# Kernel tuning notes

Measured on AMD Instinct MI355X. Metric: run time of the kernel, lower is better.

The kernel has to match this reference:

```python
import jax, jax.numpy as jnp
import numpy as np

EMBED = 768
HEADS = 12
HEAD_DIM = EMBED // HEADS
HIDDEN = 4 * EMBED
EPS = 1e-5


def setup_inputs() -> dict:
    key = jax.random.key(0)
    ks = jax.random.split(key, 12)
    s = lambda fan_in: 1.0 / np.sqrt(fan_in)
    return {
        "x": jax.random.normal(ks[0], (4, 2048, EMBED), dtype=jnp.float32),
        "ln1_g": jnp.ones((EMBED,), jnp.float32),
        "ln1_b": jnp.zeros((EMBED,), jnp.float32),
        "qkv_w": jax.random.normal(ks[1], (EMBED, 3 * EMBED), jnp.float32) * s(EMBED),
        "qkv_b": jnp.zeros((3 * EMBED,), jnp.float32),
        "proj_w": jax.random.normal(ks[2], (EMBED, EMBED), jnp.float32) * s(EMBED),
        "proj_b": jnp.zeros((EMBED,), jnp.float32),
        "ln2_g": jnp.ones((EMBED,), jnp.float32),
        "ln2_b": jnp.zeros((EMBED,), jnp.float32),
        "fc1_w": jax.random.normal(ks[3], (EMBED, HIDDEN), jnp.float32) * s(EMBED),
        "fc1_b": jnp.zeros((HIDDEN,), jnp.float32),
        "fc2_w": jax.random.normal(ks[4], (HIDDEN, EMBED), jnp.float32) * s(HIDDEN),
        "fc2_b": jnp.zeros((EMBED,), jnp.float32),
    }


def _layernorm(x, g, b):
    mu = jnp.mean(x, axis=-1, keepdims=True)
    var = jnp.var(x, axis=-1, keepdims=True)
    return (x - mu) * jax.lax.rsqrt(var + EPS) * g + b


def reference(x, ln1_g, ln1_b, qkv_w, qkv_b, proj_w, proj_b,
              ln2_g, ln2_b, fc1_w, fc1_b, fc2_w, fc2_b):
    B, N, C = x.shape
    # --- attention (pre-LN) ---
    xn = _layernorm(x, ln1_g, ln1_b)
    qkv = xn @ qkv_w + qkv_b                       # [B,N,3C]
    qkv = qkv.reshape(B, N, 3, HEADS, HEAD_DIM)
    q, k, v = jnp.moveaxis(qkv, 2, 0)              # each [B,N,H,D]
    q = jnp.swapaxes(q, 1, 2)                      # [B,H,N,D]
    k = jnp.swapaxes(k, 1, 2)
    v = jnp.swapaxes(v, 1, 2)
    scale = HEAD_DIM ** -0.5
    attn = jax.nn.softmax(jnp.einsum('bhnd,bhmd->bhnm', q, k) * scale, axis=-1)
    out = jnp.einsum('bhnm,bhmd->bhnd', attn, v)   # [B,H,N,D]
    out = jnp.swapaxes(out, 1, 2).reshape(B, N, C)
    out = out @ proj_w + proj_b
    x = x + out
    # --- MLP (pre-LN) ---
    xn2 = _layernorm(x, ln2_g, ln2_b)
    h = jax.nn.gelu(xn2 @ fc1_w + fc1_b, approximate=False)
    x = x + (h @ fc2_w + fc2_b)
    return x
```

## Files before the change

### kernel.cpp

```cpp
#include <hip/hip_runtime.h>

typedef unsigned short ushort_t;
typedef __attribute__((ext_vector_type(8))) unsigned short ushort8;
typedef __attribute__((ext_vector_type(4))) unsigned short ushort4v;
typedef __attribute__((ext_vector_type(2))) unsigned int uint2v;
typedef __attribute__((ext_vector_type(4))) float f32x4;
typedef __attribute__((ext_vector_type(8))) __bf16 bf16x8;

#define DEVFN static __device__ __forceinline__

DEVFN unsigned short f2bf(float f) {
    unsigned int u = __builtin_bit_cast(unsigned int, f);
    u += 0x7FFFu + ((u >> 16) & 1u);
    return (unsigned short)(u >> 16);
}

DEVFN bf16x8 ldsfrag(const ushort_t* p) {
    ushort8 u = *reinterpret_cast<const ushort8*>(p);
    return __builtin_bit_cast(bf16x8, u);
}

DEVFN bf16x8 ldg8(const ushort_t* p) {
    ushort8 u = *reinterpret_cast<const ushort8*>(p);
    return __builtin_bit_cast(bf16x8, u);
}

DEVFN f32x4 mfma16(bf16x8 a, bf16x8 b, f32x4 c) {
    return __builtin_amdgcn_mfma_f32_16x16x32_bf16(a, b, c, 0, 0, 0);
}

DEVFN void gl2lds16(const ushort_t* g, ushort_t* l) {
    __builtin_amdgcn_global_load_lds(
        (const __attribute__((address_space(1))) unsigned int*)g,
        (__attribute__((address_space(3))) unsigned int*)l, 16, 0, 0);
}

DEVFN unsigned int cvtpk(float lo, float hi) {
    unsigned int r;
    asm("v_cvt_pk_bf16_f32 %0, %1, %2" : "=v"(r) : "v"(lo), "v"(hi));
    return r;
}

DEVFN float gelu_fast(float v) {
    const float a = 0.7978845608f * v * fmaf(0.044715f, v * v, 1.0f);
    const float e = __builtin_amdgcn_exp2f(2.885390082f * a);
    const float th = 1.0f - 2.0f * __builtin_amdgcn_rcpf(e + 1.0f);
    return 0.5f * v * (1.0f + th);
}

__global__ __launch_bounds__(256) void prep_kernel(
    const float* __restrict__ qkv_w, const float* __restrict__ proj_w,
    const float* __restrict__ fc1_w, const float* __restrict__ fc2_w,
    ushort_t* __restrict__ qkv_wt, ushort_t* __restrict__ proj_wt,
    ushort_t* __restrict__ fc1_wt, ushort_t* __restrict__ fc2_wt,
    const float* __restrict__ x, const float* __restrict__ ln1_g,
    const float* __restrict__ ln1_b, ushort_t* __restrict__ xb) {
    __shared__ float t[32][33];
    const int bid = blockIdx.x;
    const int tid = threadIdx.x;

    if (bid >= 6912) {
        const int row = bid - 6912;
        const float* xr = x + (size_t)row * 768;
        float v0 = xr[tid], v1 = xr[tid + 256], v2 = xr[tid + 512];
        float s = v0 + v1 + v2;
        float q = v0 * v0 + v1 * v1 + v2 * v2;
        for (int d = 32; d; d >>= 1) {
            s += __shfl_down(s, d);
            q += __shfl_down(q, d);
        }
        float* red = &t[0][0];
        const int w = tid >> 6, lane = tid & 63;
        if (lane == 0) { red[w] = s; red[4 + w] = q; }
        __syncthreads();
        if (tid == 0) {
            float ts = red[0] + red[1] + red[2] + red[3];
            float tq = red[4] + red[5] + red[6] + red[7];
            float mu = ts * (1.0f / 768.0f);
            float var = tq * (1.0f / 768.0f) - mu * mu;
            red[0] = mu;
            red[1] = rsqrtf(var + 1e-5f);
        }
        __syncthreads();
        const float mu = red[0], rs = red[1];
        ushort_t* orow = xb + (size_t)row * 768;
        orow[tid]       = f2bf((v0 - mu) * rs * ln1_g[tid]       + ln1_b[tid]);
        orow[tid + 256] = f2bf((v1 - mu) * rs * ln1_g[tid + 256] + ln1_b[tid + 256]);
        orow[tid + 512] = f2bf((v2 - mu) * rs * ln1_g[tid + 512] + ln1_b[tid + 512]);
        return;
    }

    const float* in; ushort_t* out; int K, N, n0, k0;
    if (bid < 1728)      { in = qkv_w;  out = qkv_wt;  K = 768;  N = 2304;
                           n0 = (bid % 72) * 32;  k0 = (bid / 72) * 32; }
    else if (bid < 2304) { const int r = bid - 1728; in = proj_w; out = proj_wt;
                           K = 768;  N = 768;
                           n0 = (r % 24) * 32;    k0 = (r / 24) * 32; }
    else if (bid < 4608) { const int r = bid - 2304; in = fc1_w;  out = fc1_wt;
                           K = 768;  N = 3072;
                           n0 = (r % 96) * 32;    k0 = (r / 96) * 32; }
    else                 { const int r = bid - 4608; in = fc2_w;  out = fc2_wt;
                           K = 3072; N = 768;
                           n0 = (r % 24) * 32;    k0 = (r / 24) * 32; }
    const int tx = tid & 31, ty = tid >> 5;
    for (int j = 0; j < 4; j++)
        t[ty + 8 * j][tx] = in[(size_t)(k0 + ty + 8 * j) * N + n0 + tx];
    __syncthreads();
    for (int j = 0; j < 4; j++)
        out[(size_t)(n0 + ty + 8 * j) * K + k0 + tx] = f2bf(t[tx][ty + 8 * j]);
}

__global__ __launch_bounds__(256) void ln_kernel(const float* __restrict__ x,
                                                 const float* __restrict__ g,
                                                 const float* __restrict__ bta,
                                                 ushort_t* __restrict__ out) {
    const int row = blockIdx.x;
    const int tid = threadIdx.x;
    const float* xr = x + (size_t)row * 768;
    float v0 = xr[tid], v1 = xr[tid + 256], v2 = xr[tid + 512];
    float s = v0 + v1 + v2;
    float q = v0 * v0 + v1 * v1 + v2 * v2;
    for (int d = 32; d; d >>= 1) {
        s += __shfl_down(s, d);
        q += __shfl_down(q, d);
    }
    __shared__ float red[8];
    const int w = tid >> 6, lane = tid & 63;
    if (lane == 0) { red[w] = s; red[4 + w] = q; }
    __syncthreads();
    if (tid == 0) {
        float ts = red[0] + red[1] + red[2] + red[3];
        float tq = red[4] + red[5] + red[6] + red[7];
        float mu = ts * (1.0f / 768.0f);
        float var = tq * (1.0f / 768.0f) - mu * mu;
        red[0] = mu;
        red[1] = rsqrtf(var + 1e-5f);
    }
    __syncthreads();
    const float mu = red[0], rs = red[1];
    ushort_t* orow = out + (size_t)row * 768;
    orow[tid]       = f2bf((v0 - mu) * rs * g[tid]       + bta[tid]);
    orow[tid + 256] = f2bf((v1 - mu) * rs * g[tid + 256] + bta[tid + 256]);
    orow[tid + 512] = f2bf((v2 - mu) * rs * g[tid + 512] + bta[tid + 512]);
}

enum { EPI_QKV = 0, EPI_RES = 1, EPI_GELU = 2 };

template <int EPI, int BN, int BK>
__global__ __launch_bounds__(256) void gemm_kernel(
    const ushort_t* __restrict__ A, const ushort_t* __restrict__ BT,
    const float* __restrict__ bias, const float* __restrict__ resid,
    float* __restrict__ outf, ushort_t* __restrict__ outb,
    ushort_t* __restrict__ vtout, int M, int N, int K) {
    constexpr int NT = BN / 32;
    constexpr int SL = BK / 8;
    constexpr int SM = SL - 1;
    constexpr int RPI = 64 / SL;
    constexpr int AI = 128 / RPI / 4;
    constexpr int BI = BN / RPI / 4;
    __shared__ __align__(16) ushort_t As[2][128 * BK];
    __shared__ __align__(16) ushort_t Bs[2][BN * BK];
    const int id = blockIdx.x;
    const int nbn = gridDim.x >> 6;
    const int p = id >> 3;
    const int bn = p % nbn;
    const int bm = (id & 7) * 8 + p / nbn;
    const int tid = threadIdx.x;
    const int lane = tid & 63, w = tid >> 6;
    const int wm = (w >> 1) * 64, wn = (w & 1) * (BN / 2);
    const int l15 = lane & 15, l4 = lane >> 4;

    const int srow = lane / SL;
    const int scol = ((lane & SM) ^ (srow & SM)) * 8;
    const ushort_t* gA = A + (size_t)(bm * 128 + w * (AI * RPI) + srow) * K + scol;
    const ushort_t* gB = BT + (size_t)(bn * BN + w * (BI * RPI) + srow) * K + scol;

    const int swm = l15 & SM;
    int aoff[BK / 32], boff[BK / 32];
#pragma unroll
    for (int kk = 0; kk < BK / 32; kk++) {
        aoff[kk] = (wm + l15) * BK + ((((kk << 2) | l4) ^ swm) * 8);
        boff[kk] = (wn + l15) * BK + ((((kk << 2) | l4) ^ swm) * 8);
    }

    f32x4 acc[4][NT] = {};

    auto stage = [&](int k0, int buf) {
#pragma unroll
        for (int i = 0; i < AI; i++)
            gl2lds16(gA + k0 + i * RPI * K, &As[buf][(w * AI + i) * 512]);
#pragma unroll
        for (int i = 0; i < BI; i++)
            gl2lds16(gB + k0 + i * RPI * K, &Bs[buf][(w * BI + i) * 512]);
    };

    stage(0, 0);
    __syncthreads();
    int cur = 0;
    for (int k0 = 0; k0 < K; k0 += BK) {
        if (k0 + BK < K) stage(k0 + BK, cur ^ 1);
#pragma unroll
        for (int kk = 0; kk < BK / 32; kk++) {
            bf16x8 af[4], bfr[NT];
#pragma unroll
            for (int mt = 0; mt < 4; mt++)
                af[mt] = ldsfrag(As[cur] + aoff[kk] + mt * 16 * BK);
#pragma unroll
            for (int nt = 0; nt < NT; nt++)
                bfr[nt] = ldsfrag(Bs[cur] + boff[kk] + nt * 16 * BK);
#pragma unroll
            for (int mt = 0; mt < 4; mt++)
#pragma unroll
                for (int nt = 0; nt < NT; nt++)
                    acc[mt][nt] = mfma16(bfr[nt], af[mt], acc[mt][nt]);
        }
        __syncthreads();
        cur ^= 1;
    }

#pragma unroll
    for (int nt = 0; nt < NT; nt++) {
        const int gc0 = bn * BN + wn + nt * 16 + l4 * 4;
        const f32x4 bi = *reinterpret_cast<const f32x4*>(bias + gc0);
#pragma unroll
        for (int mt = 0; mt < 4; mt++) {
            const int gr = bm * 128 + wm + mt * 16 + l15;
            f32x4 v = acc[mt][nt] + bi;
            if constexpr (EPI == EPI_QKV) {
                if (gc0 < 768) v *= 0.18033688011f;
                if (gc0 >= 1536) {
                    const int d = gc0 - 1536;
                    const int h = d >> 6, dh = d & 63;
                    const int b = gr >> 11, tl = gr & 2047;
                    ushort_t* vrow = vtout + ((size_t)((b * 12 + h) * 64 + dh)) * 2048 + tl;
                    vrow[0]        = f2bf(v[0]);
                    vrow[2048]     = f2bf(v[1]);
                    vrow[2 * 2048] = f2bf(v[2]);
                    vrow[3 * 2048] = f2bf(v[3]);
                } else {
                    uint2v o;
                    o[0] = cvtpk(v[0], v[1]);
                    o[1] = cvtpk(v[2], v[3]);
                    *reinterpret_cast<uint2v*>(outb + (size_t)gr * N + gc0) = o;
                }
            } else if constexpr (EPI == EPI_RES) {
                const f32x4 rsd = *reinterpret_cast<const f32x4*>(resid + (size_t)gr * N + gc0);
                *reinterpret_cast<f32x4*>(outf + (size_t)gr * N + gc0) = v + rsd;
            } else {
                f32x4 gl;
#pragma unroll
                for (int r = 0; r < 4; r++) gl[r] = gelu_fast(v[r]);
                uint2v o;
                o[0] = cvtpk(gl[0], gl[1]);
                o[1] = cvtpk(gl[2], gl[3]);
                *reinterpret_cast<uint2v*>(outb + (size_t)gr * N + gc0) = o;
            }
        }
    }
}

__global__ __launch_bounds__(256, 4) void attn_kernel(const ushort_t* __restrict__ qkv,
                                                      const ushort_t* __restrict__ vt,
                                                      ushort_t* __restrict__ out) {
    __shared__ __align__(16) ushort_t Kb[2][4096];
    __shared__ __align__(16) ushort_t Vb[2][4096];
    __shared__ __align__(16) ushort_t Ps[4][1024];

    const int bid = blockIdx.x;
    const int nid = (bid & 7) * 192 + (bid >> 3);
    const int qt = nid & 31;
    const int bh = nid >> 5;
    const int b = bh / 12, h = bh % 12;
    const int tid = threadIdx.x;
    const int lane = tid & 63, w = tid >> 6;
    const int l15 = lane & 15, l4 = lane >> 4;

    const ushort_t* qrow = qkv + (size_t)(b * 2048 + qt * 64 + w * 16 + l15) * 2304 + h * 64;
    const bf16x8 aq0 = ldg8(qrow + l4 * 8);
    const bf16x8 aq1 = ldg8(qrow + 32 + l4 * 8);

    const int jr0 = w * 16 + (lane >> 3);
    const int jr1 = jr0 + 8;
    const int c0 = ((lane & 7) ^ (jr0 & 7)) * 8;
    const int c1 = ((lane & 7) ^ (jr1 & 7)) * 8;
    const ushort_t* kg0 = qkv + (size_t)(b * 2048 + jr0) * 2304 + 768 + h * 64 + c0;
    const ushort_t* kg1 = qkv + (size_t)(b * 2048 + jr1) * 2304 + 768 + h * 64 + c1;
    const ushort_t* vg0 = vt + (size_t)(bh * 64 + jr0) * 2048 + c0;
    const ushort_t* vg1 = vt + (size_t)(bh * 64 + jr1) * 2048 + c1;

    const int sw7 = l15 & 7;
    const int ka0 = l15 * 64 + ((l4 ^ sw7) * 8);
    const int ka1 = l15 * 64 + (((4 + l4) ^ sw7) * 8);

    ushort_t* const psw = Ps[w];
    const int pw_m = l15 & 14;
    int pwoff[4];
#pragma unroll
    for (int jt = 0; jt < 4; jt++) pwoff[jt] = l15 * 64 + (((jt * 4 + l4) ^ pw_m) * 4);
    const int pr0 = l15 * 64 + (((2 * l4) ^ pw_m) * 4);
    const int pr1 = l15 * 64 + (((8 + 2 * l4) ^ pw_m) * 4);

    float lrun = 0.f;
    f32x4 oacc[4] = {};

    gl2lds16(kg0, &Kb[0][w * 1024]);
    gl2lds16(kg1, &Kb[0][w * 1024 + 512]);
    gl2lds16(vg0, &Vb[0][w * 1024]);
    gl2lds16(vg1, &Vb[0][w * 1024 + 512]);
    __syncthreads();

    for (int kt = 0; kt < 32; kt++) {
        const int cur = kt & 1;
        if (kt < 31) {
            const size_t ko = (size_t)(kt + 1) * 64 * 2304;
            const int vo = (kt + 1) * 64;
            gl2lds16(kg0 + ko, &Kb[cur ^ 1][w * 1024]);
            gl2lds16(kg1 + ko, &Kb[cur ^ 1][w * 1024 + 512]);
            gl2lds16(vg0 + vo, &Vb[cur ^ 1][w * 1024]);
            gl2lds16(vg1 + vo, &Vb[cur ^ 1][w * 1024 + 512]);
        }
        const ushort_t* kb = Kb[cur];
        const ushort_t* vb = Vb[cur];

        f32x4 st[4];
        __builtin_amdgcn_s_setprio(1);
#pragma unroll
        for (int jt = 0; jt < 4; jt++) {
            f32x4 z = {};
            z = mfma16(ldsfrag(kb + ka0 + jt * 1024), aq0, z);
            z = mfma16(ldsfrag(kb + ka1 + jt * 1024), aq1, z);
            st[jt] = z;
        }
        __builtin_amdgcn_s_setprio(0);

        float rs = 0.f;
#pragma unroll
        for (int jt = 0; jt < 4; jt++) {
            const float p0 = __builtin_amdgcn_exp2f(st[jt][0]);
            const float p1 = __builtin_amdgcn_exp2f(st[jt][1]);
            const float p2 = __builtin_amdgcn_exp2f(st[jt][2]);
            const float p3 = __builtin_amdgcn_exp2f(st[jt][3]);
            rs += (p0 + p1) + (p2 + p3);
            uint2v pw;
            pw[0] = cvtpk(p0, p1);
            pw[1] = cvtpk(p2, p3);
            *reinterpret_cast<uint2v*>(psw + pwoff[jt]) = pw;
        }
        lrun += rs;

        const bf16x8 pf0 = ldsfrag(psw + pr0);
        const bf16x8 pf1 = ldsfrag(psw + pr1);

        __builtin_amdgcn_s_setprio(1);
#pragma unroll
        for (int dt = 0; dt < 4; dt++) {
            const bf16x8 vf0 = ldsfrag(vb + ka0 + dt * 1024);
            const bf16x8 vf1 = ldsfrag(vb + ka1 + dt * 1024);
            oacc[dt] = mfma16(vf0, pf0, oacc[dt]);
            oacc[dt] = mfma16(vf1, pf1, oacc[dt]);
        }
        __builtin_amdgcn_s_setprio(0);
        __syncthreads();
    }

    lrun += __shfl_xor(lrun, 16);
    lrun += __shfl_xor(lrun, 32);
    const float linv = __builtin_amdgcn_rcpf(lrun);

    ushort_t* orow = out + (size_t)(b * 2048 + qt * 64 + w * 16 + l15) * 768 + h * 64 + l4 * 4;
#pragma unroll
    for (int dt = 0; dt < 4; dt++) {
        ushort4v o;
#pragma unroll
        for (int r = 0; r < 4; r++) o[r] = f2bf(oacc[dt][r] * linv);
        *reinterpret_cast<ushort4v*>(orow + dt * 16) = o;
    }
}

extern "C" void kernel_launch(void* const* d_in, const int* in_sizes, int n_in,
                              void* d_out, int out_size, void* d_ws, size_t ws_size,
                              hipStream_t stream) {
    const float* x      = (const float*)d_in[0];
    const float* ln1_g  = (const float*)d_in[1];
    const float* ln1_b  = (const float*)d_in[2];
    const float* qkv_w  = (const float*)d_in[3];
    const float* qkv_b  = (const float*)d_in[4];
    const float* proj_w = (const float*)d_in[5];
    const float* proj_b = (const float*)d_in[6];
    const float* ln2_g  = (const float*)d_in[7];
    const float* ln2_b  = (const float*)d_in[8];
    const float* fc1_w  = (const float*)d_in[9];
    const float* fc1_b  = (const float*)d_in[10];
    const float* fc2_w  = (const float*)d_in[11];
    const float* fc2_b  = (const float*)d_in[12];
    float* out = (float*)d_out;

    char* ws = (char*)d_ws;
    ushort_t* qkv_wt  = (ushort_t*)(ws);
    ushort_t* proj_wt = (ushort_t*)(ws + 3538944);
    ushort_t* fc1_wt  = (ushort_t*)(ws + 4718592);
    ushort_t* fc2_wt  = (ushort_t*)(ws + 9437184);
    ushort_t* xb      = (ushort_t*)(ws + 14155776);
    ushort_t* aob     = (ushort_t*)(ws + 26738688);
    ushort_t* qkvb    = (ushort_t*)(ws + 39321600);
    ushort_t* vtb     = (ushort_t*)(ws + 77070336);
    ushort_t* hb      = (ushort_t*)(ws + 39321600);

    dim3 blk(256);

    prep_kernel<<<dim3(15104), blk, 0, stream>>>(qkv_w, proj_w, fc1_w, fc2_w,
                                                 qkv_wt, proj_wt, fc1_wt, fc2_wt,
                                                 x, ln1_g, ln1_b, xb);
    gemm_kernel<EPI_QKV, 128, 32><<<dim3(18 * 64), blk, 0, stream>>>(
        xb, qkv_wt, qkv_b, nullptr, nullptr, qkvb, vtb, 8192, 2304, 768);
    attn_kernel<<<dim3(1536), blk, 0, stream>>>(qkvb, vtb, aob);
    gemm_kernel<EPI_RES, 64, 64><<<dim3(12 * 64), blk, 0, stream>>>(
        aob, proj_wt, proj_b, x, out, nullptr, nullptr, 8192, 768, 768);
    ln_kernel<<<8192, blk, 0, stream>>>(out, ln2_g, ln2_b, xb);
    gemm_kernel<EPI_GELU, 128, 32><<<dim3(24 * 64), blk, 0, stream>>>(
        xb, fc1_wt, fc1_b, nullptr, nullptr, hb, nullptr, 8192, 3072, 768);
    gemm_kernel<EPI_RES, 64, 64><<<dim3(12 * 64), blk, 0, stream>>>(
        hb, fc2_wt, fc2_b, out, out, nullptr, nullptr, 8192, 768, 3072);
}
```

Measured before the change: 282.6 us.

## Process two query tiles per attention block to reuse K/V loads

Each attention block now handles 128 query rows (two 64-row sub-tiles) instead of 64, so every K/V tile staged in LDS feeds twice as many MFMAs. The grid is halved to 768 blocks and launch bounds drop to 3 waves-per-SIMD occupancy to make room for the doubled accumulators and P buffers. The aim is to cut global K/V traffic and the sync overhead per unit of work. The cost is more register pressure, lower occupancy and fewer blocks for 256 CUs, which may leave some CUs underfilled.

```diff
diff --git a/kernel.cpp b/kernel.cpp
--- a/kernel.cpp
+++ b/kernel.cpp
@@ -259,25 +259,28 @@
     }
 }
 
-__global__ __launch_bounds__(256, 4) void attn_kernel(const ushort_t* __restrict__ qkv,
+__global__ __launch_bounds__(256, 3) void attn_kernel(const ushort_t* __restrict__ qkv,
                                                       const ushort_t* __restrict__ vt,
                                                       ushort_t* __restrict__ out) {
     __shared__ __align__(16) ushort_t Kb[2][4096];
     __shared__ __align__(16) ushort_t Vb[2][4096];
-    __shared__ __align__(16) ushort_t Ps[4][1024];
+    __shared__ __align__(16) ushort_t Ps[4][2][1024];
 
     const int bid = blockIdx.x;
-    const int nid = (bid & 7) * 192 + (bid >> 3);
-    const int qt = nid & 31;
-    const int bh = nid >> 5;
+    const int nid = (bid & 7) * 96 + (bid >> 3);
+    const int qt = nid & 15;
+    const int bh = nid >> 4;
     const int b = bh / 12, h = bh % 12;
     const int tid = threadIdx.x;
     const int lane = tid & 63, w = tid >> 6;
     const int l15 = lane & 15, l4 = lane >> 4;
 
-    const ushort_t* qrow = qkv + (size_t)(b * 2048 + qt * 64 + w * 16 + l15) * 2304 + h * 64;
-    const bf16x8 aq0 = ldg8(qrow + l4 * 8);
-    const bf16x8 aq1 = ldg8(qrow + 32 + l4 * 8);
+    const ushort_t* qrowA = qkv + (size_t)(b * 2048 + qt * 128 + w * 16 + l15) * 2304 + h * 64;
+    const ushort_t* qrowB = qrowA + (size_t)64 * 2304;
+    const bf16x8 aqA0 = ldg8(qrowA + l4 * 8);
+    const bf16x8 aqA1 = ldg8(qrowA + 32 + l4 * 8);
+    const bf16x8 aqB0 = ldg8(qrowB + l4 * 8);
+    const bf16x8 aqB1 = ldg8(qrowB + 32 + l4 * 8);
 
     const int jr0 = w * 16 + (lane >> 3);
     const int jr1 = jr0 + 8;
@@ -292,7 +295,8 @@
     const int ka0 = l15 * 64 + ((l4 ^ sw7) * 8);
     const int ka1 = l15 * 64 + (((4 + l4) ^ sw7) * 8);
 
-    ushort_t* const psw = Ps[w];
+    ushort_t* const psA = Ps[w][0];
+    ushort_t* const psB = Ps[w][1];
     const int pw_m = l15 & 14;
     int pwoff[4];
 #pragma unroll
@@ -300,8 +304,8 @@
     const int pr0 = l15 * 64 + (((2 * l4) ^ pw_m) * 4);
     const int pr1 = l15 * 64 + (((8 + 2 * l4) ^ pw_m) * 4);
 
-    float lrun = 0.f;
-    f32x4 oacc[4] = {};
+    float lrunA = 0.f, lrunB = 0.f;
+    f32x4 oaccA[4] = {}, oaccB[4] = {};
 
     gl2lds16(kg0, &Kb[0][w * 1024]);
     gl2lds16(kg1, &Kb[0][w * 1024 + 512]);
@@ -322,58 +326,85 @@
         const ushort_t* kb = Kb[cur];
         const ushort_t* vb = Vb[cur];
 
-        f32x4 st[4];
+        f32x4 stA[4], stB[4];
         __builtin_amdgcn_s_setprio(1);
 #pragma unroll
         for (int jt = 0; jt < 4; jt++) {
-            f32x4 z = {};
-            z = mfma16(ldsfrag(kb + ka0 + jt * 1024), aq0, z);
-            z = mfma16(ldsfrag(kb + ka1 + jt * 1024), aq1, z);
-            st[jt] = z;
+            const bf16x8 kf0 = ldsfrag(kb + ka0 + jt * 1024);
+            const bf16x8 kf1 = ldsfrag(kb + ka1 + jt * 1024);
+            f32x4 zA = {}, zB = {};
+            zA = mfma16(kf0, aqA0, zA);
+            zB = mfma16(kf0, aqB0, zB);
+            zA = mfma16(kf1, aqA1, zA);
+            zB = mfma16(kf1, aqB1, zB);
+            stA[jt] = zA;
+            stB[jt] = zB;
         }
         __builtin_amdgcn_s_setprio(0);
 
-        float rs = 0.f;
+        float rsA = 0.f, rsB = 0.f;
 #pragma unroll
         for (int jt = 0; jt < 4; jt++) {
-            const float p0 = __builtin_amdgcn_exp2f(st[jt][0]);
-            const float p1 = __builtin_amdgcn_exp2f(st[jt][1]);
-            const float p2 = __builtin_amdgcn_exp2f(st[jt][2]);
-            const float p3 = __builtin_amdgcn_exp2f(st[jt][3]);
-            rs += (p0 + p1) + (p2 + p3);
-            uint2v pw;
-            pw[0] = cvtpk(p0, p1);
-            pw[1] = cvtpk(p2, p3);
-            *reinterpret_cast<uint2v*>(psw + pwoff[jt]) = pw;
-        }
-        lrun += rs;
-
-        const bf16x8 pf0 = ldsfrag(psw + pr0);
-        const bf16x8 pf1 = ldsfrag(psw + pr1);
+            const float a0 = __builtin_amdgcn_exp2f(stA[jt][0]);
+            const float a1 = __builtin_amdgcn_exp2f(stA[jt][1]);
+            const float a2 = __builtin_amdgcn_exp2f(stA[jt][2]);
+            const float a3 = __builtin_amdgcn_exp2f(stA[jt][3]);
+            rsA += (a0 + a1) + (a2 + a3);
+            uint2v pwA;
+            pwA[0] = cvtpk(a0, a1);
+            pwA[1] = cvtpk(a2, a3);
+            *reinterpret_cast<uint2v*>(psA + pwoff[jt]) = pwA;
+            const float b0 = __builtin_amdgcn_exp2f(stB[jt][0]);
+            const float b1 = __builtin_amdgcn_exp2f(stB[jt][1]);
+            const float b2 = __builtin_amdgcn_exp2f(stB[jt][2]);
+            const float b3 = __builtin_amdgcn_exp2f(stB[jt][3]);
+            rsB += (b0 + b1) + (b2 + b3);
+            uint2v pwB;
+            pwB[0] = cvtpk(b0, b1);
+            pwB[1] = cvtpk(b2, b3);
+            *reinterpret_cast<uint2v*>(psB + pwoff[jt]) = pwB;
+        }
+        lrunA += rsA;
+        lrunB += rsB;
+
+        const bf16x8 pfA0 = ldsfrag(psA + pr0);
+        const bf16x8 pfA1 = ldsfrag(psA + pr1);
+        const bf16x8 pfB0 = ldsfrag(psB + pr0);
+        const bf16x8 pfB1 = ldsfrag(psB + pr1);
 
         __builtin_amdgcn_s_setprio(1);
 #pragma unroll
         for (int dt = 0; dt < 4; dt++) {
             const bf16x8 vf0 = ldsfrag(vb + ka0 + dt * 1024);
             const bf16x8 vf1 = ldsfrag(vb + ka1 + dt * 1024);
-            oacc[dt] = mfma16(vf0, pf0, oacc[dt]);
-            oacc[dt] = mfma16(vf1, pf1, oacc[dt]);
+            oaccA[dt] = mfma16(vf0, pfA0, oaccA[dt]);
+            oaccB[dt] = mfma16(vf0, pfB0, oaccB[dt]);
+            oaccA[dt] = mfma16(vf1, pfA1, oaccA[dt]);
+            oaccB[dt] = mfma16(vf1, pfB1, oaccB[dt]);
         }
         __builtin_amdgcn_s_setprio(0);
         __syncthreads();
     }
 
-    lrun += __shfl_xor(lrun, 16);
-    lrun += __shfl_xor(lrun, 32);
-    const float linv = __builtin_amdgcn_rcpf(lrun);
-
-    ushort_t* orow = out + (size_t)(b * 2048 + qt * 64 + w * 16 + l15) * 768 + h * 64 + l4 * 4;
+    lrunA += __shfl_xor(lrunA, 16);
+    lrunA += __shfl_xor(lrunA, 32);
+    lrunB += __shfl_xor(lrunB, 16);
+    lrunB += __shfl_xor(lrunB, 32);
+    const float linvA = __builtin_amdgcn_rcpf(lrunA);
+    const float linvB = __builtin_amdgcn_rcpf(lrunB);
+
+    ushort_t* orowA = out + (size_t)(b * 2048 + qt * 128 + w * 16 + l15) * 768 + h * 64 + l4 * 4;
+    ushort_t* orowB = orowA + (size_t)64 * 768;
 #pragma unroll
     for (int dt = 0; dt < 4; dt++) {
-        ushort4v o;
-#pragma unroll
-        for (int r = 0; r < 4; r++) o[r] = f2bf(oacc[dt][r] * linv);
-        *reinterpret_cast<ushort4v*>(orow + dt * 16) = o;
+        ushort4v oA, oB;
+#pragma unroll
+        for (int r = 0; r < 4; r++) {
+            oA[r] = f2bf(oaccA[dt][r] * linvA);
+            oB[r] = f2bf(oaccB[dt][r] * linvB);
+        }
+        *reinterpret_cast<ushort4v*>(orowA + dt * 16) = oA;
+        *reinterpret_cast<ushort4v*>(orowB + dt * 16) = oB;
     }
 }
 
@@ -413,7 +444,7 @@
                                                  x, ln1_g, ln1_b, xb);
     gemm_kernel<EPI_QKV, 128, 32><<<dim3(18 * 64), blk, 0, stream>>>(
         xb, qkv_wt, qkv_b, nullptr, nullptr, qkvb, vtb, 8192, 2304, 768);
-    attn_kernel<<<dim3(1536), blk, 0, stream>>>(qkvb, vtb, aob);
+    attn_kernel<<<dim3(768), blk, 0, stream>>>(qkvb, vtb, aob);
     gemm_kernel<EPI_RES, 64, 64><<<dim3(12 * 64), blk, 0, stream>>>(
         aob, proj_wt, proj_b, x, out, nullptr, nullptr, 8192, 768, 768);
     ln_kernel<<<8192, blk, 0, stream>>>(out, ln2_g, ln2_b, xb);
```

After: 269.3 us. 4.7% less time.

## Switch attention to 32x32x16 MFMA with register-resident P via permlane swap

Applied to the files above, without the earlier changes.

The attention kernel moves from 16x16x32 to 32x32x16 bf16 MFMA tiles, so each wave now owns 32 query rows and a block covers 128 queries, halving the grid. The softmax probabilities are repacked in registers with v_permlane32_swap to form the B operand of the PV matmul, which removes the per-wave LDS staging buffer and its write/read round trip. Each K/V tile loaded into LDS is reused across twice as many queries, cutting LDS and global traffic per query. In exchange there are fewer blocks (768) to cover the CUs and more accumulator registers per wave, which may reduce occupancy.

```diff
diff --git a/kernel.cpp b/kernel.cpp
--- a/kernel.cpp
+++ b/kernel.cpp
@@ -4,7 +4,9 @@
 typedef __attribute__((ext_vector_type(8))) unsigned short ushort8;
 typedef __attribute__((ext_vector_type(4))) unsigned short ushort4v;
 typedef __attribute__((ext_vector_type(2))) unsigned int uint2v;
+typedef __attribute__((ext_vector_type(4))) unsigned int uint4v;
 typedef __attribute__((ext_vector_type(4))) float f32x4;
+typedef __attribute__((ext_vector_type(16))) float f32x16;
 typedef __attribute__((ext_vector_type(8))) __bf16 bf16x8;
 
 #define DEVFN static __device__ __forceinline__
@@ -29,6 +31,10 @@
     return __builtin_amdgcn_mfma_f32_16x16x32_bf16(a, b, c, 0, 0, 0);
 }
 
+DEVFN f32x16 mfma32(bf16x8 a, bf16x8 b, f32x16 c) {
+    return __builtin_amdgcn_mfma_f32_32x32x16_bf16(a, b, c, 0, 0, 0);
+}
+
 DEVFN void gl2lds16(const ushort_t* g, ushort_t* l) {
     __builtin_amdgcn_global_load_lds(
         (const __attribute__((address_space(1))) unsigned int*)g,
@@ -39,6 +45,10 @@
     unsigned int r;
     asm("v_cvt_pk_bf16_f32 %0, %1, %2" : "=v"(r) : "v"(lo), "v"(hi));
     return r;
+}
+
+DEVFN void permswap(unsigned int& a, unsigned int& b) {
+    asm("v_permlane32_swap_b32 %0, %1" : "+v"(a), "+v"(b));
 }
 
 DEVFN float gelu_fast(float v) {
@@ -264,20 +274,21 @@
                                                       ushort_t* __restrict__ out) {
     __shared__ __align__(16) ushort_t Kb[2][4096];
     __shared__ __align__(16) ushort_t Vb[2][4096];
-    __shared__ __align__(16) ushort_t Ps[4][1024];
 
     const int bid = blockIdx.x;
-    const int nid = (bid & 7) * 192 + (bid >> 3);
-    const int qt = nid & 31;
-    const int bh = nid >> 5;
+    const int nid = (bid & 7) * 96 + (bid >> 3);
+    const int qt = nid & 15;
+    const int bh = nid >> 4;
     const int b = bh / 12, h = bh % 12;
     const int tid = threadIdx.x;
     const int lane = tid & 63, w = tid >> 6;
-    const int l15 = lane & 15, l4 = lane >> 4;
-
-    const ushort_t* qrow = qkv + (size_t)(b * 2048 + qt * 64 + w * 16 + l15) * 2304 + h * 64;
-    const bf16x8 aq0 = ldg8(qrow + l4 * 8);
-    const bf16x8 aq1 = ldg8(qrow + 32 + l4 * 8);
+    const int l31 = lane & 31, hi = lane >> 5;
+
+    const ushort_t* qrow = qkv + (size_t)(b * 2048 + qt * 128 + w * 32 + l31) * 2304
+                               + h * 64 + hi * 8;
+    bf16x8 qf[4];
+#pragma unroll
+    for (int ks = 0; ks < 4; ks++) qf[ks] = ldg8(qrow + ks * 16);
 
     const int jr0 = w * 16 + (lane >> 3);
     const int jr1 = jr0 + 8;
@@ -288,20 +299,13 @@
     const ushort_t* vg0 = vt + (size_t)(bh * 64 + jr0) * 2048 + c0;
     const ushort_t* vg1 = vt + (size_t)(bh * 64 + jr1) * 2048 + c1;
 
-    const int sw7 = l15 & 7;
-    const int ka0 = l15 * 64 + ((l4 ^ sw7) * 8);
-    const int ka1 = l15 * 64 + (((4 + l4) ^ sw7) * 8);
-
-    ushort_t* const psw = Ps[w];
-    const int pw_m = l15 & 14;
-    int pwoff[4];
-#pragma unroll
-    for (int jt = 0; jt < 4; jt++) pwoff[jt] = l15 * 64 + (((jt * 4 + l4) ^ pw_m) * 4);
-    const int pr0 = l15 * 64 + (((2 * l4) ^ pw_m) * 4);
-    const int pr1 = l15 * 64 + (((8 + 2 * l4) ^ pw_m) * 4);
+    const int sw7 = lane & 7;
+    int fo[4];
+#pragma unroll
+    for (int s = 0; s < 4; s++) fo[s] = l31 * 64 + ((((s << 1) | hi) ^ sw7) * 8);
 
     float lrun = 0.f;
-    f32x4 oacc[4] = {};
+    f32x16 oacc0 = {}, oacc1 = {};
 
     gl2lds16(kg0, &Kb[0][w * 1024]);
     gl2lds16(kg1, &Kb[0][w * 1024 + 512]);
@@ -322,58 +326,72 @@
         const ushort_t* kb = Kb[cur];
         const ushort_t* vb = Vb[cur];
 
-        f32x4 st[4];
+        f32x16 sA = {}, sB = {};
         __builtin_amdgcn_s_setprio(1);
 #pragma unroll
-        for (int jt = 0; jt < 4; jt++) {
-            f32x4 z = {};
-            z = mfma16(ldsfrag(kb + ka0 + jt * 1024), aq0, z);
-            z = mfma16(ldsfrag(kb + ka1 + jt * 1024), aq1, z);
-            st[jt] = z;
+        for (int ks = 0; ks < 4; ks++) {
+            const bf16x8 k0 = ldsfrag(kb + fo[ks]);
+            const bf16x8 k1 = ldsfrag(kb + fo[ks] + 2048);
+            sA = mfma32(k0, qf[ks], sA);
+            sB = mfma32(k1, qf[ks], sB);
         }
         __builtin_amdgcn_s_setprio(0);
 
+        bf16x8 pf[4];
         float rs = 0.f;
 #pragma unroll
-        for (int jt = 0; jt < 4; jt++) {
-            const float p0 = __builtin_amdgcn_exp2f(st[jt][0]);
-            const float p1 = __builtin_amdgcn_exp2f(st[jt][1]);
-            const float p2 = __builtin_amdgcn_exp2f(st[jt][2]);
-            const float p3 = __builtin_amdgcn_exp2f(st[jt][3]);
-            rs += (p0 + p1) + (p2 + p3);
-            uint2v pw;
-            pw[0] = cvtpk(p0, p1);
-            pw[1] = cvtpk(p2, p3);
-            *reinterpret_cast<uint2v*>(psw + pwoff[jt]) = pw;
+        for (int blk = 0; blk < 2; blk++) {
+            const f32x16& sv = blk ? sB : sA;
+            unsigned int wd[8];
+#pragma unroll
+            for (int g = 0; g < 4; g++) {
+                const float e0 = __builtin_amdgcn_exp2f(sv[4 * g + 0]);
+                const float e1 = __builtin_amdgcn_exp2f(sv[4 * g + 1]);
+                const float e2 = __builtin_amdgcn_exp2f(sv[4 * g + 2]);
+                const float e3 = __builtin_amdgcn_exp2f(sv[4 * g + 3]);
+                rs += (e0 + e1) + (e2 + e3);
+                wd[2 * g]     = cvtpk(e0, e1);
+                wd[2 * g + 1] = cvtpk(e2, e3);
+            }
+            permswap(wd[0], wd[2]);
+            permswap(wd[1], wd[3]);
+            permswap(wd[4], wd[6]);
+            permswap(wd[5], wd[7]);
+            uint4v flo, fhi;
+            flo[0] = wd[0]; flo[1] = wd[1]; flo[2] = wd[2]; flo[3] = wd[3];
+            fhi[0] = wd[4]; fhi[1] = wd[5]; fhi[2] = wd[6]; fhi[3] = wd[7];
+            pf[2 * blk]     = __builtin_bit_cast(bf16x8, flo);
+            pf[2 * blk + 1] = __builtin_bit_cast(bf16x8, fhi);
         }
         lrun += rs;
 
-        const bf16x8 pf0 = ldsfrag(psw + pr0);
-        const bf16x8 pf1 = ldsfrag(psw + pr1);
-
         __builtin_amdgcn_s_setprio(1);
 #pragma unroll
-        for (int dt = 0; dt < 4; dt++) {
-            const bf16x8 vf0 = ldsfrag(vb + ka0 + dt * 1024);
-            const bf16x8 vf1 = ldsfrag(vb + ka1 + dt * 1024);
-            oacc[dt] = mfma16(vf0, pf0, oacc[dt]);
-            oacc[dt] = mfma16(vf1, pf1, oacc[dt]);
+        for (int s = 0; s < 4; s++) {
+            const bf16x8 v0 = ldsfrag(vb + fo[s]);
+            const bf16x8 v1 = ldsfrag(vb + fo[s] + 2048);
+            oacc0 = mfma32(v0, pf[s], oacc0);
+            oacc1 = mfma32(v1, pf[s], oacc1);
         }
         __builtin_amdgcn_s_setprio(0);
         __syncthreads();
     }
 
-    lrun += __shfl_xor(lrun, 16);
     lrun += __shfl_xor(lrun, 32);
     const float linv = __builtin_amdgcn_rcpf(lrun);
 
-    ushort_t* orow = out + (size_t)(b * 2048 + qt * 64 + w * 16 + l15) * 768 + h * 64 + l4 * 4;
-#pragma unroll
-    for (int dt = 0; dt < 4; dt++) {
-        ushort4v o;
-#pragma unroll
-        for (int r = 0; r < 4; r++) o[r] = f2bf(oacc[dt][r] * linv);
-        *reinterpret_cast<ushort4v*>(orow + dt * 16) = o;
+    ushort_t* orow = out + (size_t)(b * 2048 + qt * 128 + w * 32 + l31) * 768 + h * 64;
+#pragma unroll
+    for (int dblk = 0; dblk < 2; dblk++) {
+        const f32x16& ov = dblk ? oacc1 : oacc0;
+#pragma unroll
+        for (int g = 0; g < 4; g++) {
+            const int d0 = dblk * 32 + 8 * g + 4 * hi;
+            ushort4v o;
+#pragma unroll
+            for (int r = 0; r < 4; r++) o[r] = f2bf(ov[4 * g + r] * linv);
+            *reinterpret_cast<ushort4v*>(orow + d0) = o;
+        }
     }
 }
 
@@ -413,7 +431,7 @@
                                                  x, ln1_g, ln1_b, xb);
     gemm_kernel<EPI_QKV, 128, 32><<<dim3(18 * 64), blk, 0, stream>>>(
         xb, qkv_wt, qkv_b, nullptr, nullptr, qkvb, vtb, 8192, 2304, 768);
-    attn_kernel<<<dim3(1536), blk, 0, stream>>>(qkvb, vtb, aob);
+    attn_kernel<<<dim3(768), blk, 0, stream>>>(qkvb, vtb, aob);
     gemm_kernel<EPI_RES, 64, 64><<<dim3(12 * 64), blk, 0, stream>>>(
         aob, proj_wt, proj_b, x, out, nullptr, nullptr, 8192, 768, 768);
     ln_kernel<<<8192, blk, 0, stream>>>(out, ln2_g, ln2_b, xb);
```

After: 268.9 us. 4.8% less time.
